# Optimization experiments

Measured on AMD Instinct MI355X. Metric: run time of the kernel, lower is better.

The kernel has to match this reference:

```python
import jax, jax.numpy as jnp
import numpy as np

N = 100000   # nodes
E = 3200000  # edges (avg degree 32)
G = 512      # graphs in batch
F_IN = 10
H = 30


def setup_inputs() -> dict:
    key = jax.random.key(0)
    ks = jax.random.split(key, 14)
    x = jax.random.normal(ks[0], (N, F_IN), dtype=jnp.float32)
    edge_index = jax.random.randint(ks[1], (2, E), 0, N, dtype=jnp.int64)
    batch = jnp.sort(jax.random.randint(ks[2], (N,), 0, G, dtype=jnp.int64))
    edge_weights = jnp.ones((E,), dtype=jnp.float32)
    s = 0.1
    W1 = jax.random.normal(ks[3], (F_IN, H), jnp.float32) * s
    b1 = jnp.zeros((H,), jnp.float32)
    W2 = jax.random.normal(ks[4], (H, H), jnp.float32) * s
    b2 = jnp.zeros((H,), jnp.float32)
    W3 = jax.random.normal(ks[5], (H, H), jnp.float32) * s
    b3 = jnp.zeros((H,), jnp.float32)
    LW1 = jax.random.normal(ks[6], (H, 10), jnp.float32) * s
    Lb1 = jnp.zeros((10,), jnp.float32)
    LW2 = jax.random.normal(ks[7], (10, 2), jnp.float32) * s
    Lb2 = jnp.zeros((2,), jnp.float32)
    return dict(x=x, edge_index=edge_index, batch=batch, edge_weights=edge_weights,
                W1=W1, b1=b1, W2=W2, b2=b2, W3=W3, b3=b3,
                LW1=LW1, Lb1=Lb1, LW2=LW2, Lb2=Lb2)


def reference(x, edge_index, batch, edge_weights, W1, b1, W2, b2, W3, b3, LW1, Lb1, LW2, Lb2):
    n = x.shape[0]
    row, col = edge_index[0], edge_index[1]
    # PyG gcn_norm: add self-loops with weight 1, symmetric normalization
    loop = jnp.arange(n)
    row_f = jnp.concatenate([row, loop])
    col_f = jnp.concatenate([col, loop])
    w_f = jnp.concatenate([edge_weights, jnp.ones((n,), edge_weights.dtype)])
    deg = jax.ops.segment_sum(w_f, col_f, num_segments=n)
    dis = jnp.where(deg > 0, jax.lax.rsqrt(jnp.where(deg > 0, deg, 1.0)), 0.0)
    norm = dis[row_f] * w_f * dis[col_f]  # [E+N]

    def gcn(h, W, b):
        h = h @ W  # [N, out]
        agg = jax.ops.segment_sum(norm[:, None] * h[row_f], col_f, num_segments=n)
        return agg + b

    h = jax.nn.relu(gcn(x, W1, b1))
    h = jax.nn.relu(gcn(h, W2, b2))
    h = jax.nn.relu(gcn(h, W3, b3))  # embedding [N, 30]
    pooled = jax.ops.segment_max(h, batch, num_segments=G)  # [G, 30]
    out = jax.nn.relu(pooled @ LW1 + Lb1) @ LW2 + Lb2  # [G, 2]
    return out
```

## Files before the change

### kernel.cpp

```cpp
#include <hip/hip_runtime.h>
#include <hip/hip_bf16.h>


#define WG 256
#define CAP 9216
#define T_EDGES 16384

__global__ void k_init(int* bcur, float* pooled, int nb16, int pooledN) {
    int i = blockIdx.x * blockDim.x + threadIdx.x;
    if (i < nb16) bcur[i] = 0;
    if (i < pooledN) pooled[i] = 0.0f;
}

__global__ __launch_bounds__(1024)
void k_bucket(const int* __restrict__ row, const int* __restrict__ col,
              const float* __restrict__ w,
              int* bcur, int2* __restrict__ buck, int E, int NB) {
    __shared__ int hist[512];
    __shared__ int base[512];
    int tid = threadIdx.x;
    for (int i = tid; i < NB; i += 1024) hist[i] = 0;
    __syncthreads();
    int start = blockIdx.x * T_EDGES;
    int end = min(start + T_EDGES, E);
    for (int i = start + tid; i < end; i += 1024)
        atomicAdd(&hist[col[i] >> 8], 1);
    __syncthreads();
    for (int i = tid; i < NB; i += 1024) {
        int h = hist[i];
        base[i] = (h > 0) ? atomicAdd(&bcur[i * 16], h) : 0;
        hist[i] = 0;
    }
    __syncthreads();
    for (int i = start + tid; i < end; i += 1024) {
        int c = col[i];
        int b = c >> 8;
        int off = atomicAdd(&hist[b], 1);
        int pos = base[b] + off;
        if (pos < CAP) {
            int2 pk;
            pk.x = (c & 255) | (row[i] << 8);
            pk.y = __float_as_int(w[i]);
            buck[(size_t)b * CAP + pos] = pk;
        }
    }
}

__global__ __launch_bounds__(1024)
void k_fuse(const int* __restrict__ bcur, const int2* __restrict__ buck,
            float* __restrict__ dis, int* __restrict__ ptr,
            int2* __restrict__ csr, int N, int NB) {
    __shared__ int lc[256];
    __shared__ float lw[256];
    __shared__ int sh[256];
    __shared__ int cur[256];
    __shared__ int sb[512];
    int b = blockIdx.x;
    int tid = threadIdx.x;
    if (tid < 512) sb[tid] = (tid < NB) ? min(bcur[tid * 16], CAP) : 0;
    if (tid < 256) { lc[tid] = 0; lw[tid] = 0.0f; }
    __syncthreads();
    for (int off = 1; off < 512; off <<= 1) {
        int v = (tid < 512 && tid >= off) ? sb[tid - off] : 0;
        __syncthreads();
        if (tid < 512) sb[tid] += v;
        __syncthreads();
    }
    int m = min(bcur[b * 16], CAP);
    int bbase = sb[b] - m;
    if (b == 0 && tid == 0) ptr[N] = sb[511];
    const int2* bp = buck + (size_t)b * CAP;
    for (int i = tid; i < m; i += 1024) {
        int2 pk = bp[i];
        int lcol = pk.x & 255;
        atomicAdd(&lc[lcol], 1);
        atomicAdd(&lw[lcol], __int_as_float(pk.y));
    }
    __syncthreads();
    int lcnt = 0;
    if (tid < 256) { lcnt = lc[tid]; sh[tid] = lcnt; }
    __syncthreads();
    for (int off = 1; off < 256; off <<= 1) {
        int t = (tid >= off && tid < 256) ? sh[tid - off] : 0;
        __syncthreads();
        if (tid < 256) sh[tid] += t;
        __syncthreads();
    }
    int node = (b << 8) + tid;
    if (tid < 256) {
        int base = bbase + sh[tid] - lcnt;
        cur[tid] = base;
        if (node < N) {
            ptr[node] = base;
            float d = 1.0f + lw[tid];
            dis[node] = (d > 0.0f) ? (1.0f / sqrtf(d)) : 0.0f;
        }
    }
    __syncthreads();
    for (int i = tid; i < m; i += 1024) {
        int2 pk = bp[i];
        int lcol = pk.x & 255;
        int pos = atomicAdd(&cur[lcol], 1);
        int2 rec;
        rec.x = (int)(((unsigned)pk.x) >> 8);
        rec.y = pk.y;
        csr[pos] = rec;
    }
}

__global__ void k_stage(const float* __restrict__ x, const float* __restrict__ dis,
                        float* __restrict__ xp, int n) {
    int gid = blockIdx.x * blockDim.x + threadIdx.x;
    int node = gid >> 4, f = gid & 15;
    if (node < n)
        xp[(size_t)node * 16 + f] = (f < 10) ? dis[node] * x[(size_t)node * 10 + f] : 0.0f;
}

__global__ void k_agg16(const float* __restrict__ xp, const float* __restrict__ dis,
                        const int* __restrict__ ptr, const int2* __restrict__ csr,
                        float* __restrict__ y, int n) {
    int wid = (blockIdx.x * blockDim.x + threadIdx.x) >> 6;
    int lane = threadIdx.x & 63;
    if (wid >= n) return;
    int f = lane & 15;
    int q = lane >> 4;
    int s = ptr[wid];
    int e = ptr[wid + 1];
    float acc = 0.0f;
    for (int base = s; base < e; base += 32) {
        int idxv = 0; float nrmv = 0.0f;
        int src = base + lane;
        if (lane < 32 && src < e) {
            int2 v = csr[src];
            idxv = v.x;
            nrmv = __int_as_float(v.y);
        }
#pragma unroll
        for (int j = 0; j < 8; j++) {
            int sl = 4 * j + q;
            int r = __shfl(idxv, sl, 64);
            float w = __shfl(nrmv, sl, 64);
            acc += w * xp[(size_t)r * 16 + f];
        }
    }
    acc += __shfl_xor(acc, 16, 64);
    acc += __shfl_xor(acc, 32, 64);
    float dc = dis[wid];
    float r = dc * (acc + xp[(size_t)wid * 16 + f]);
    if (lane < 16) y[(size_t)wid * 16 + f] = r;
}

__global__ __launch_bounds__(256)
void k_lin1(const float* __restrict__ y, const float* __restrict__ W1,
            const float* __restrict__ b1, const float* __restrict__ W2,
            const float* __restrict__ dis, float* __restrict__ out, int n) {
    __shared__ float W1s[10 * 32];
    __shared__ float W2s[30 * 32];
    __shared__ float b1s[32];
    __shared__ float ys[8][16];
    __shared__ float hs[8][32];
    int tid = threadIdx.x;
    for (int i = tid; i < 10 * 32; i += 256) { int k = i >> 5, f = i & 31; W1s[i] = (f < 30) ? W1[k * 30 + f] : 0.0f; }
    for (int i = tid; i < 30 * 32; i += 256) { int k = i >> 5, f = i & 31; W2s[i] = (f < 30) ? W2[k * 30 + f] : 0.0f; }
    if (tid < 32) b1s[tid] = (tid < 30) ? b1[tid] : 0.0f;
    int n8 = tid >> 5, f = tid & 31;
    int node = blockIdx.x * 8 + n8;
    __syncthreads();
    if (node < n && f < 16) ys[n8][f] = y[(size_t)node * 16 + f];
    __syncthreads();
    if (node < n) {
        float h = b1s[f];
#pragma unroll
        for (int k = 0; k < 10; k++) h += ys[n8][k] * W1s[k * 32 + f];
        h = fmaxf(h, 0.0f);
        if (f >= 30) h = 0.0f;
        hs[n8][f] = h;
    }
    __syncthreads();
    if (node < n) {
        float o = 0.0f;
#pragma unroll
        for (int k = 0; k < 30; k++) o += hs[n8][k] * W2s[k * 32 + f];
        out[(size_t)node * 32 + f] = o * dis[node];
    }
}

__global__ void k_matmul30(const float* __restrict__ in,
                           const float* __restrict__ W, const float* __restrict__ dis,
                           float* __restrict__ out, int n) {
    __shared__ float Ws[30 * 30];
    for (int idx = threadIdx.x; idx < 30 * 30; idx += blockDim.x) Ws[idx] = W[idx];
    __syncthreads();
    int gid = blockIdx.x * blockDim.x + threadIdx.x;
    int node = gid >> 5;
    int f = gid & 31;
    if (node < n) {
        float acc = 0.0f;
        if (f < 30) {
            const float* ip = in + (size_t)node * 32;
#pragma unroll
            for (int k = 0; k < 30; k++) acc += ip[k] * Ws[k * 30 + f];
            acc *= dis[node];
        }
        out[(size_t)node * 32 + f] = acc;
    }
}

__global__ void k_agg(const float* __restrict__ hw, const float* __restrict__ dis,
                      const int* __restrict__ ptr, const int2* __restrict__ csr,
                      const float* __restrict__ bias,
                      float* __restrict__ out, int n) {
    int wid = (blockIdx.x * blockDim.x + threadIdx.x) >> 6;
    int lane = threadIdx.x & 63;
    if (wid >= n) return;
    int f = lane & 31;
    int half = lane >> 5;
    int s = ptr[wid];
    int e = ptr[wid + 1];
    float acc = 0.0f;
    for (int base = s; base < e; base += 32) {
        int idxv = 0; float nrmv = 0.0f;
        int src = base + lane;
        if (lane < 32 && src < e) {
            int2 v = csr[src];
            idxv = v.x;
            nrmv = __int_as_float(v.y);
        }
#pragma unroll
        for (int j = 0; j < 16; j++) {
            int sl = 2 * j + half;
            int r = __shfl(idxv, sl, 64);
            float w = __shfl(nrmv, sl, 64);
            acc += w * hw[(size_t)r * 32 + f];
        }
    }
    acc += __shfl_xor(acc, 32, 64);
    float dc = dis[wid];
    float r = dc * (acc + hw[(size_t)wid * 32 + f]);
    if (half == 0 && f < 30) {
        r += bias[f];
        out[(size_t)wid * 32 + f] = fmaxf(r, 0.0f);
    }
}

__global__ void k_pool(const float* __restrict__ h, const int* __restrict__ batch,
                       float* pooled, int n) {
    int gid = blockIdx.x * blockDim.x + threadIdx.x;
    int chunk = gid >> 5;
    int f = gid & 31;
    int n0 = chunk * 64;
    if (n0 >= n || f >= 30) return;
    int end = min(n0 + 64, n);
    int curg = batch[n0];
    float m = 0.0f;
    for (int i = n0; i < end; i++) {
        int g = batch[i];
        if (g != curg) {
            atomicMax((int*)&pooled[curg * 32 + f], __float_as_int(m));
            m = 0.0f;
            curg = g;
        }
        m = fmaxf(m, h[(size_t)i * 32 + f]);
    }
    atomicMax((int*)&pooled[curg * 32 + f], __float_as_int(m));
}

__global__ void k_mlp(const float* __restrict__ pooled,
                      const float* __restrict__ LW1, const float* __restrict__ Lb1,
                      const float* __restrict__ LW2, const float* __restrict__ Lb2,
                      float* __restrict__ out, int G) {
    int g = blockIdx.x * blockDim.x + threadIdx.x;
    if (g >= G) return;
    float p[30];
#pragma unroll
    for (int k = 0; k < 30; k++) p[k] = pooled[g * 32 + k];
    float o0 = Lb2[0], o1 = Lb2[1];
#pragma unroll
    for (int j = 0; j < 10; j++) {
        float hj = Lb1[j];
#pragma unroll
        for (int k = 0; k < 30; k++) hj += p[k] * LW1[k * 10 + j];
        hj = fmaxf(hj, 0.0f);
        o0 += hj * LW2[j * 2 + 0];
        o1 += hj * LW2[j * 2 + 1];
    }
    out[g * 2 + 0] = o0;
    out[g * 2 + 1] = o1;
}

extern "C" void kernel_launch(void* const* d_in, const int* in_sizes, int n_in,
                              void* d_out, int out_size, void* d_ws, size_t ws_size,
                              hipStream_t stream) {
    const float* x     = (const float*)d_in[0];
    const int*   ei    = (const int*)d_in[1];
    const int*   batch = (const int*)d_in[2];
    const float* ew    = (const float*)d_in[3];
    const float* W1 = (const float*)d_in[4];  const float* b1  = (const float*)d_in[5];
    const float* W2 = (const float*)d_in[6];  const float* b2  = (const float*)d_in[7];
    const float* W3 = (const float*)d_in[8];  const float* b3  = (const float*)d_in[9];
    const float* LW1 = (const float*)d_in[10]; const float* Lb1 = (const float*)d_in[11];
    const float* LW2 = (const float*)d_in[12]; const float* Lb2 = (const float*)d_in[13];
    float* out = (float*)d_out;

    const int N = in_sizes[2];
    const int E = in_sizes[3];
    const int G = out_size / 2;
    const int* row = ei;
    const int* col = ei + E;

    const int NB = (N + 255) >> 8;

    char* p = (char*)d_ws;
    auto carve = [&](size_t bytes) -> void* {
        void* r = (void*)p;
        p += (bytes + 255) & ~(size_t)255;
        return r;
    };
    int*   ptr       = (int*)carve((size_t)(N + 1) * 4);
    float* dis       = (float*)carve((size_t)N * 4);
    int*   bcur      = (int*)carve((size_t)NB * 16 * 4);
    int2*  csr       = (int2*)carve((size_t)E * 8);
    size_t buckBytes = (size_t)NB * CAP * 8;
    size_t featBytes = (size_t)N * 32 * 4 * 2;
    char*  regionA   = (char*)carve(buckBytes > featBytes ? buckBytes : featBytes);
    int2*  buck      = (int2*)regionA;
    float* bufA      = (float*)regionA;
    float* xp        = (float*)regionA;
    float* y16       = (float*)(regionA + (size_t)N * 16 * 4);
    float* bufB      = (float*)(regionA + (size_t)N * 32 * 4);
    float* pooled    = (float*)carve((size_t)G * 32 * 4);

    int initN = (NB * 16 > G * 32) ? NB * 16 : G * 32;

    k_init<<<(initN + WG - 1) / WG, WG, 0, stream>>>(bcur, pooled, NB * 16, G * 32);
    k_bucket<<<(E + T_EDGES - 1) / T_EDGES, 1024, 0, stream>>>(row, col, ew, bcur, buck, E, NB);
    k_fuse<<<NB, 1024, 0, stream>>>(bcur, buck, dis, ptr, csr, N, NB);

    int agg_grid = (int)(((size_t)N * 64 + WG - 1) / WG);
    int mm_grid  = (int)(((size_t)N * 32 + WG - 1) / WG);

    k_stage<<<(int)(((size_t)N * 16 + WG - 1) / WG), WG, 0, stream>>>(x, dis, xp, N);
    k_agg16<<<agg_grid, WG, 0, stream>>>(xp, dis, ptr, csr, y16, N);
    k_lin1<<<(N + 7) / 8, 256, 0, stream>>>(y16, W1, b1, W2, dis, bufB, N);
    k_agg<<<agg_grid, WG, 0, stream>>>(bufB, dis, ptr, csr, b2, bufA, N);
    k_matmul30<<<mm_grid, WG, 0, stream>>>(bufA, W3, dis, bufB, N);
    k_agg<<<agg_grid, WG, 0, stream>>>(bufB, dis, ptr, csr, b3, bufA, N);

    int pool_grid = (int)((((size_t)(N + 63) / 64) * 32 + WG - 1) / WG);
    k_pool<<<pool_grid, WG, 0, stream>>>(bufA, batch, pooled, N);
    k_mlp<<<(G + WG - 1) / WG, WG, 0, stream>>>(pooled, LW1, Lb1, LW2, Lb2, out, G);
}
```

Measured before the change: 424.9 us.

## Pack multiple destination nodes per wavefront in GCN aggregation kernels

The aggregation kernels now assign 4 nodes (16-feature layer) or 2 nodes (32-feature layers) to each 64-lane wavefront instead of one node per wave. This removes the idle half or quarter lanes and the cross-lane reduction, and shrinks the grid. Four independent accumulators are added to raise memory-level parallelism in the gather loop. The cost is that nodes sharing a wave iterate to the largest degree among them, so some lanes sit idle on imbalanced degrees.

```diff
diff --git a/kernel.cpp b/kernel.cpp
--- a/kernel.cpp
+++ b/kernel.cpp
@@ -121,33 +121,41 @@
                         float* __restrict__ y, int n) {
     int wid = (blockIdx.x * blockDim.x + threadIdx.x) >> 6;
     int lane = threadIdx.x & 63;
-    if (wid >= n) return;
     int f = lane & 15;
-    int q = lane >> 4;
-    int s = ptr[wid];
-    int e = ptr[wid + 1];
-    float acc = 0.0f;
-    for (int base = s; base < e; base += 32) {
+    int laneq = lane & 48;
+    int node = 4 * wid + (lane >> 4);
+    bool valid = node < n;
+    int s = 0, e = 0;
+    if (valid) { s = ptr[node]; e = ptr[node + 1]; }
+    int len = e - s;
+    int m01 = max(__shfl(len, 0, 64), __shfl(len, 16, 64));
+    int m23 = max(__shfl(len, 32, 64), __shfl(len, 48, 64));
+    int maxlen = max(m01, m23);
+    float a0 = 0.0f, a1 = 0.0f, a2 = 0.0f, a3 = 0.0f;
+    for (int off = 0; off < maxlen; off += 16) {
         int idxv = 0; float nrmv = 0.0f;
-        int src = base + lane;
-        if (lane < 32 && src < e) {
-            int2 v = csr[src];
+        if (off + f < len) {
+            int2 v = csr[s + off + f];
             idxv = v.x;
             nrmv = __int_as_float(v.y);
         }
 #pragma unroll
-        for (int j = 0; j < 8; j++) {
-            int sl = 4 * j + q;
-            int r = __shfl(idxv, sl, 64);
-            float w = __shfl(nrmv, sl, 64);
-            acc += w * xp[(size_t)r * 16 + f];
-        }
-    }
-    acc += __shfl_xor(acc, 16, 64);
-    acc += __shfl_xor(acc, 32, 64);
-    float dc = dis[wid];
-    float r = dc * (acc + xp[(size_t)wid * 16 + f]);
-    if (lane < 16) y[(size_t)wid * 16 + f] = r;
+        for (int j = 0; j < 16; j += 4) {
+            int r0 = __shfl(idxv, laneq | j, 64);       float w0 = __shfl(nrmv, laneq | j, 64);
+            int r1 = __shfl(idxv, laneq | (j + 1), 64); float w1 = __shfl(nrmv, laneq | (j + 1), 64);
+            int r2 = __shfl(idxv, laneq | (j + 2), 64); float w2 = __shfl(nrmv, laneq | (j + 2), 64);
+            int r3 = __shfl(idxv, laneq | (j + 3), 64); float w3 = __shfl(nrmv, laneq | (j + 3), 64);
+            a0 = fmaf(w0, xp[(size_t)r0 * 16 + f], a0);
+            a1 = fmaf(w1, xp[(size_t)r1 * 16 + f], a1);
+            a2 = fmaf(w2, xp[(size_t)r2 * 16 + f], a2);
+            a3 = fmaf(w3, xp[(size_t)r3 * 16 + f], a3);
+        }
+    }
+    if (valid) {
+        float acc = (a0 + a1) + (a2 + a3);
+        float r = dis[node] * (acc + xp[(size_t)node * 16 + f]);
+        y[(size_t)node * 16 + f] = r;
+    }
 }
 
 __global__ __launch_bounds__(256)
@@ -212,34 +220,38 @@
                       float* __restrict__ out, int n) {
     int wid = (blockIdx.x * blockDim.x + threadIdx.x) >> 6;
     int lane = threadIdx.x & 63;
-    if (wid >= n) return;
     int f = lane & 31;
-    int half = lane >> 5;
-    int s = ptr[wid];
-    int e = ptr[wid + 1];
-    float acc = 0.0f;
-    for (int base = s; base < e; base += 32) {
+    int lane32 = lane & 32;
+    int node = 2 * wid + (lane >> 5);
+    bool valid = node < n;
+    int s = 0, e = 0;
+    if (valid) { s = ptr[node]; e = ptr[node + 1]; }
+    int len = e - s;
+    int maxlen = max(__shfl(len, 0, 64), __shfl(len, 32, 64));
+    float a0 = 0.0f, a1 = 0.0f, a2 = 0.0f, a3 = 0.0f;
+    for (int off = 0; off < maxlen; off += 32) {
         int idxv = 0; float nrmv = 0.0f;
-        int src = base + lane;
-        if (lane < 32 && src < e) {
-            int2 v = csr[src];
+        if (off + f < len) {
+            int2 v = csr[s + off + f];
             idxv = v.x;
             nrmv = __int_as_float(v.y);
         }
 #pragma unroll
-        for (int j = 0; j < 16; j++) {
-            int sl = 2 * j + half;
-            int r = __shfl(idxv, sl, 64);
-            float w = __shfl(nrmv, sl, 64);
-            acc += w * hw[(size_t)r * 32 + f];
-        }
-    }
-    acc += __shfl_xor(acc, 32, 64);
-    float dc = dis[wid];
-    float r = dc * (acc + hw[(size_t)wid * 32 + f]);
-    if (half == 0 && f < 30) {
-        r += bias[f];
-        out[(size_t)wid * 32 + f] = fmaxf(r, 0.0f);
+        for (int j = 0; j < 32; j += 4) {
+            int r0 = __shfl(idxv, lane32 | j, 64);       float w0 = __shfl(nrmv, lane32 | j, 64);
+            int r1 = __shfl(idxv, lane32 | (j + 1), 64); float w1 = __shfl(nrmv, lane32 | (j + 1), 64);
+            int r2 = __shfl(idxv, lane32 | (j + 2), 64); float w2 = __shfl(nrmv, lane32 | (j + 2), 64);
+            int r3 = __shfl(idxv, lane32 | (j + 3), 64); float w3 = __shfl(nrmv, lane32 | (j + 3), 64);
+            a0 = fmaf(w0, hw[(size_t)r0 * 32 + f], a0);
+            a1 = fmaf(w1, hw[(size_t)r1 * 32 + f], a1);
+            a2 = fmaf(w2, hw[(size_t)r2 * 32 + f], a2);
+            a3 = fmaf(w3, hw[(size_t)r3 * 32 + f], a3);
+        }
+    }
+    if (valid && f < 30) {
+        float acc = (a0 + a1) + (a2 + a3);
+        float r = dis[node] * (acc + hw[(size_t)node * 32 + f]);
+        out[(size_t)node * 32 + f] = fmaxf(r + bias[f], 0.0f);
     }
 }
 
@@ -336,11 +348,12 @@
     k_bucket<<<(E + T_EDGES - 1) / T_EDGES, 1024, 0, stream>>>(row, col, ew, bcur, buck, E, NB);
     k_fuse<<<NB, 1024, 0, stream>>>(bcur, buck, dis, ptr, csr, N, NB);
 
-    int agg_grid = (int)(((size_t)N * 64 + WG - 1) / WG);
-    int mm_grid  = (int)(((size_t)N * 32 + WG - 1) / WG);
+    int agg_grid   = (int)(((size_t)((N + 1) / 2) * 64 + WG - 1) / WG);
+    int agg16_grid = (int)(((size_t)((N + 3) / 4) * 64 + WG - 1) / WG);
+    int mm_grid    = (int)(((size_t)N * 32 + WG - 1) / WG);
 
     k_stage<<<(int)(((size_t)N * 16 + WG - 1) / WG), WG, 0, stream>>>(x, dis, xp, N);
-    k_agg16<<<agg_grid, WG, 0, stream>>>(xp, dis, ptr, csr, y16, N);
+    k_agg16<<<agg16_grid, WG, 0, stream>>>(xp, dis, ptr, csr, y16, N);
     k_lin1<<<(N + 7) / 8, 256, 0, stream>>>(y16, W1, b1, W2, dis, bufB, N);
     k_agg<<<agg_grid, WG, 0, stream>>>(bufB, dis, ptr, csr, b2, bufA, N);
     k_matmul30<<<mm_grid, WG, 0, stream>>>(bufA, W3, dis, bufB, N);
```

Measured after the change: 424.4 us. No clear change (-0.1%).

## Store gathered node features in fp16 and gather with 16-byte vector loads

Applied to the files above, without the earlier changes.

Intermediate node features that are gathered per edge (staged input and the transformed hidden features) are now stored as fp16 instead of fp32. The aggregation kernels are restructured so each lane loads 8 halfs with one 16-byte load for a different edge, accumulates 8 features in fp32 registers, and reduces across lanes with xor-shuffles at the end. This is meant to halve the bytes and cut the number of load instructions in the edge gathers. The cost is reduced precision in the stored features and more cross-lane reduction work.

```diff
diff --git a/kernel.cpp b/kernel.cpp
--- a/kernel.cpp
+++ b/kernel.cpp
@@ -1,10 +1,16 @@
 #include <hip/hip_runtime.h>
 #include <hip/hip_bf16.h>
+#include <hip/hip_fp16.h>
 
 
 #define WG 256
 #define CAP 9216
 #define T_EDGES 16384
+
+__device__ __forceinline__ float2 cvt2(unsigned u) {
+    __half2 h = *reinterpret_cast<__half2*>(&u);
+    return __half22float2(h);
+}
 
 __global__ void k_init(int* bcur, float* pooled, int nb16, int pooledN) {
     int i = blockIdx.x * blockDim.x + threadIdx.x;
@@ -109,51 +115,63 @@
 }
 
 __global__ void k_stage(const float* __restrict__ x, const float* __restrict__ dis,
-                        float* __restrict__ xp, int n) {
+                        __half* __restrict__ xp, int n) {
     int gid = blockIdx.x * blockDim.x + threadIdx.x;
     int node = gid >> 4, f = gid & 15;
     if (node < n)
-        xp[(size_t)node * 16 + f] = (f < 10) ? dis[node] * x[(size_t)node * 10 + f] : 0.0f;
-}
-
-__global__ void k_agg16(const float* __restrict__ xp, const float* __restrict__ dis,
-                        const int* __restrict__ ptr, const int2* __restrict__ csr,
-                        float* __restrict__ y, int n) {
+        xp[(size_t)node * 16 + f] = __float2half((f < 10) ? dis[node] * x[(size_t)node * 10 + f] : 0.0f);
+}
+
+__global__ __launch_bounds__(256)
+void k_agg16(const __half* __restrict__ xp, const float* __restrict__ dis,
+             const int* __restrict__ ptr, const int2* __restrict__ csr,
+             float* __restrict__ y, int n) {
     int wid = (blockIdx.x * blockDim.x + threadIdx.x) >> 6;
     int lane = threadIdx.x & 63;
     if (wid >= n) return;
-    int f = lane & 15;
-    int q = lane >> 4;
+    int esub = lane >> 1;
+    int qh = lane & 1;
     int s = ptr[wid];
-    int e = ptr[wid + 1];
-    float acc = 0.0f;
-    for (int base = s; base < e; base += 32) {
+    int len = ptr[wid + 1] - s;
+    float acc[8];
+#pragma unroll
+    for (int k = 0; k < 8; k++) acc[k] = 0.0f;
+    for (int off = 0; off < len; off += 32) {
         int idxv = 0; float nrmv = 0.0f;
-        int src = base + lane;
-        if (lane < 32 && src < e) {
-            int2 v = csr[src];
+        if (lane < 32 && off + lane < len) {
+            int2 v = csr[s + off + lane];
             idxv = v.x;
             nrmv = __int_as_float(v.y);
         }
-#pragma unroll
-        for (int j = 0; j < 8; j++) {
-            int sl = 4 * j + q;
-            int r = __shfl(idxv, sl, 64);
-            float w = __shfl(nrmv, sl, 64);
-            acc += w * xp[(size_t)r * 16 + f];
-        }
-    }
-    acc += __shfl_xor(acc, 16, 64);
-    acc += __shfl_xor(acc, 32, 64);
-    float dc = dis[wid];
-    float r = dc * (acc + xp[(size_t)wid * 16 + f]);
-    if (lane < 16) y[(size_t)wid * 16 + f] = r;
+        int r = __shfl(idxv, esub, 64);
+        float w = __shfl(nrmv, esub, 64);
+        uint4 U = *reinterpret_cast<const uint4*>(xp + (size_t)r * 16 + qh * 8);
+        float2 f0 = cvt2(U.x), f1 = cvt2(U.y), f2 = cvt2(U.z), f3 = cvt2(U.w);
+        acc[0] = fmaf(w, f0.x, acc[0]); acc[1] = fmaf(w, f0.y, acc[1]);
+        acc[2] = fmaf(w, f1.x, acc[2]); acc[3] = fmaf(w, f1.y, acc[3]);
+        acc[4] = fmaf(w, f2.x, acc[4]); acc[5] = fmaf(w, f2.y, acc[5]);
+        acc[6] = fmaf(w, f3.x, acc[6]); acc[7] = fmaf(w, f3.y, acc[7]);
+    }
+#pragma unroll
+    for (int m = 2; m <= 32; m <<= 1) {
+#pragma unroll
+        for (int k = 0; k < 8; k++) acc[k] += __shfl_xor(acc[k], m, 64);
+    }
+    if (lane < 2) {
+        float dc = dis[wid];
+        uint4 S = *reinterpret_cast<const uint4*>(xp + (size_t)wid * 16 + lane * 8);
+        float2 s0 = cvt2(S.x), s1 = cvt2(S.y), s2 = cvt2(S.z), s3 = cvt2(S.w);
+        float sf[8] = { s0.x, s0.y, s1.x, s1.y, s2.x, s2.y, s3.x, s3.y };
+#pragma unroll
+        for (int k = 0; k < 8; k++)
+            y[(size_t)wid * 16 + lane * 8 + k] = dc * (acc[k] + sf[k]);
+    }
 }
 
 __global__ __launch_bounds__(256)
 void k_lin1(const float* __restrict__ y, const float* __restrict__ W1,
             const float* __restrict__ b1, const float* __restrict__ W2,
-            const float* __restrict__ dis, float* __restrict__ out, int n) {
+            const float* __restrict__ dis, __half* __restrict__ out, int n) {
     __shared__ float W1s[10 * 32];
     __shared__ float W2s[30 * 32];
     __shared__ float b1s[32];
@@ -181,13 +199,13 @@
         float o = 0.0f;
 #pragma unroll
         for (int k = 0; k < 30; k++) o += hs[n8][k] * W2s[k * 32 + f];
-        out[(size_t)node * 32 + f] = o * dis[node];
+        out[(size_t)node * 32 + f] = __float2half(o * dis[node]);
     }
 }
 
 __global__ void k_matmul30(const float* __restrict__ in,
                            const float* __restrict__ W, const float* __restrict__ dis,
-                           float* __restrict__ out, int n) {
+                           __half* __restrict__ out, int n) {
     __shared__ float Ws[30 * 30];
     for (int idx = threadIdx.x; idx < 30 * 30; idx += blockDim.x) Ws[idx] = W[idx];
     __syncthreads();
@@ -202,44 +220,75 @@
             for (int k = 0; k < 30; k++) acc += ip[k] * Ws[k * 30 + f];
             acc *= dis[node];
         }
-        out[(size_t)node * 32 + f] = acc;
-    }
-}
-
-__global__ void k_agg(const float* __restrict__ hw, const float* __restrict__ dis,
-                      const int* __restrict__ ptr, const int2* __restrict__ csr,
-                      const float* __restrict__ bias,
-                      float* __restrict__ out, int n) {
+        out[(size_t)node * 32 + f] = __float2half(acc);
+    }
+}
+
+__global__ __launch_bounds__(256)
+void k_agg(const __half* __restrict__ hw, const float* __restrict__ dis,
+           const int* __restrict__ ptr, const int2* __restrict__ csr,
+           const float* __restrict__ bias,
+           float* __restrict__ out, int n) {
     int wid = (blockIdx.x * blockDim.x + threadIdx.x) >> 6;
     int lane = threadIdx.x & 63;
     if (wid >= n) return;
-    int f = lane & 31;
-    int half = lane >> 5;
+    int esub = lane >> 2;
+    int q = lane & 3;
     int s = ptr[wid];
-    int e = ptr[wid + 1];
-    float acc = 0.0f;
-    for (int base = s; base < e; base += 32) {
+    int len = ptr[wid + 1] - s;
+    float acc[8];
+#pragma unroll
+    for (int k = 0; k < 8; k++) acc[k] = 0.0f;
+    for (int off = 0; off < len; off += 32) {
         int idxv = 0; float nrmv = 0.0f;
-        int src = base + lane;
-        if (lane < 32 && src < e) {
-            int2 v = csr[src];
+        if (lane < 32 && off + lane < len) {
+            int2 v = csr[s + off + lane];
             idxv = v.x;
             nrmv = __int_as_float(v.y);
         }
-#pragma unroll
-        for (int j = 0; j < 16; j++) {
-            int sl = 2 * j + half;
-            int r = __shfl(idxv, sl, 64);
-            float w = __shfl(nrmv, sl, 64);
-            acc += w * hw[(size_t)r * 32 + f];
-        }
-    }
-    acc += __shfl_xor(acc, 32, 64);
-    float dc = dis[wid];
-    float r = dc * (acc + hw[(size_t)wid * 32 + f]);
-    if (half == 0 && f < 30) {
-        r += bias[f];
-        out[(size_t)wid * 32 + f] = fmaxf(r, 0.0f);
+        int rA = __shfl(idxv, esub, 64);
+        float wA = __shfl(nrmv, esub, 64);
+        uint4 UA = *reinterpret_cast<const uint4*>(hw + (size_t)rA * 32 + q * 8);
+        if (off + 16 < len) {
+            int rB = __shfl(idxv, 16 + esub, 64);
+            float wB = __shfl(nrmv, 16 + esub, 64);
+            uint4 UB = *reinterpret_cast<const uint4*>(hw + (size_t)rB * 32 + q * 8);
+            float2 a0 = cvt2(UA.x), a1 = cvt2(UA.y), a2 = cvt2(UA.z), a3 = cvt2(UA.w);
+            acc[0] = fmaf(wA, a0.x, acc[0]); acc[1] = fmaf(wA, a0.y, acc[1]);
+            acc[2] = fmaf(wA, a1.x, acc[2]); acc[3] = fmaf(wA, a1.y, acc[3]);
+            acc[4] = fmaf(wA, a2.x, acc[4]); acc[5] = fmaf(wA, a2.y, acc[5]);
+            acc[6] = fmaf(wA, a3.x, acc[6]); acc[7] = fmaf(wA, a3.y, acc[7]);
+            float2 b0 = cvt2(UB.x), b1 = cvt2(UB.y), b2 = cvt2(UB.z), b3 = cvt2(UB.w);
+            acc[0] = fmaf(wB, b0.x, acc[0]); acc[1] = fmaf(wB, b0.y, acc[1]);
+            acc[2] = fmaf(wB, b1.x, acc[2]); acc[3] = fmaf(wB, b1.y, acc[3]);
+            acc[4] = fmaf(wB, b2.x, acc[4]); acc[5] = fmaf(wB, b2.y, acc[5]);
+            acc[6] = fmaf(wB, b3.x, acc[6]); acc[7] = fmaf(wB, b3.y, acc[7]);
+        } else {
+            float2 a0 = cvt2(UA.x), a1 = cvt2(UA.y), a2 = cvt2(UA.z), a3 = cvt2(UA.w);
+            acc[0] = fmaf(wA, a0.x, acc[0]); acc[1] = fmaf(wA, a0.y, acc[1]);
+            acc[2] = fmaf(wA, a1.x, acc[2]); acc[3] = fmaf(wA, a1.y, acc[3]);
+            acc[4] = fmaf(wA, a2.x, acc[4]); acc[5] = fmaf(wA, a2.y, acc[5]);
+            acc[6] = fmaf(wA, a3.x, acc[6]); acc[7] = fmaf(wA, a3.y, acc[7]);
+        }
+    }
+#pragma unroll
+    for (int m = 4; m <= 32; m <<= 1) {
+#pragma unroll
+        for (int k = 0; k < 8; k++) acc[k] += __shfl_xor(acc[k], m, 64);
+    }
+    if (lane < 4) {
+        float dc = dis[wid];
+        uint4 S = *reinterpret_cast<const uint4*>(hw + (size_t)wid * 32 + lane * 8);
+        float2 s0 = cvt2(S.x), s1 = cvt2(S.y), s2 = cvt2(S.z), s3 = cvt2(S.w);
+        float sf[8] = { s0.x, s0.y, s1.x, s1.y, s2.x, s2.y, s3.x, s3.y };
+#pragma unroll
+        for (int k = 0; k < 8; k++) {
+            int f = lane * 8 + k;
+            if (f < 30) {
+                float r = dc * (acc[k] + sf[k]) + bias[f];
+                out[(size_t)wid * 32 + f] = fmaxf(r, 0.0f);
+            }
+        }
     }
 }
 
@@ -325,9 +374,9 @@
     char*  regionA   = (char*)carve(buckBytes > featBytes ? buckBytes : featBytes);
     int2*  buck      = (int2*)regionA;
     float* bufA      = (float*)regionA;
-    float* xp        = (float*)regionA;
-    float* y16       = (float*)(regionA + (size_t)N * 16 * 4);
-    float* bufB      = (float*)(regionA + (size_t)N * 32 * 4);
+    __half* xp       = (__half*)regionA;
+    float* y16       = (float*)(regionA + (size_t)N * 16 * 2);
+    __half* bufB     = (__half*)(regionA + (size_t)N * 32 * 4);
     float* pooled    = (float*)carve((size_t)G * 32 * 4);
 
     int initN = (NB * 16 > G * 32) ? NB * 16 : G * 32;
```

Result: slower. 433.6 us (+2.1%).
